# Kernel tuning notes

Hardware: AMD Instinct MI355X
Metric: run time of the kernel (lower is better)

## Reference

```python
import jax, jax.numpy as jnp
import numpy as np

EPS = 1e-3  # keras LayerNormalization default epsilon


def _layernorm(x, gamma, beta):
    mu = jnp.mean(x, axis=-1, keepdims=True)
    var = jnp.mean(jnp.square(x - mu), axis=-1, keepdims=True)
    return (x - mu) * jax.lax.rsqrt(var + EPS) * gamma + beta


def setup_inputs() -> dict:
    key = jax.random.key(0)
    B, T, D, H = 8, 2048, 192, 3
    KD = D           # TalkingHeadsAttention(key_dim=dim, value_dim=dim)
    HID = 4 * D      # mlp_ratio = 4.0
    ks = jax.random.split(key, 12)
    s_in = 0.02
    inp = {
        "x": jax.random.normal(ks[0], (B, T, D), jnp.float32),
        # norm1 / norm2
        "gamma1": jnp.ones((D,), jnp.float32),
        "beta1": jnp.zeros((D,), jnp.float32),
        "gamma2": jnp.ones((D,), jnp.float32),
        "beta2": jnp.zeros((D,), jnp.float32),
        # attention projections (qkv_bias=False -> no biases)
        "wq": jax.random.normal(ks[1], (D, H, KD), jnp.float32) * s_in,
        "wk": jax.random.normal(ks[2], (D, H, KD), jnp.float32) * s_in,
        "wv": jax.random.normal(ks[3], (D, H, KD), jnp.float32) * s_in,
        "wo": jax.random.normal(ks[4], (H, KD, D), jnp.float32) * s_in,
        # talking-heads mixing matrices [H, H]
        "pre_w": jnp.eye(H, dtype=jnp.float32) + jax.random.normal(ks[5], (H, H), jnp.float32) * 0.02,
        "post_w": jnp.eye(H, dtype=jnp.float32) + jax.random.normal(ks[6], (H, H), jnp.float32) * 0.02,
        # MLP (bias=True)
        "w1": jax.random.normal(ks[7], (D, HID), jnp.float32) * s_in,
        "b1": jnp.zeros((HID,), jnp.float32),
        "w2": jax.random.normal(ks[8], (HID, D), jnp.float32) * s_in,
        "b2": jnp.zeros((D,), jnp.float32),
    }
    return inp


def reference(x, gamma1, beta1, gamma2, beta2, wq, wk, wv, wo, pre_w, post_w, w1, b1, w2, b2):
    KD = wq.shape[-1]
    # --- pre-norm + talking-heads attention ---
    n = _layernorm(x, gamma1, beta1)                      # [B,T,D]
    q = jnp.einsum("btd,dhk->bthk", n, wq)               # [B,T,H,KD]
    k = jnp.einsum("bsd,dhk->bshk", n, wk)
    v = jnp.einsum("bsd,dhk->bshk", n, wv)
    scores = jnp.einsum("bthk,bshk->bhts", q, k) / jnp.sqrt(jnp.asarray(KD, x.dtype))
    scores = jnp.einsum("bhts,hg->bgts", scores, pre_w)   # pre-softmax head mix
    probs = jax.nn.softmax(scores, axis=-1)
    probs = jnp.einsum("bhts,hg->bgts", probs, post_w)    # post-softmax head mix
    ctx = jnp.einsum("bhts,bshk->bthk", probs, v)         # [B,T,H,KD]
    attn_out = jnp.einsum("bthk,hkd->btd", ctx, wo)       # [B,T,D]
    x = x + attn_out                                      # ls1/drop_path1 are Identity
    # --- pre-norm + MLP ---
    n2 = _layernorm(x, gamma2, beta2)
    h = jax.nn.gelu(n2 @ w1 + b1, approximate=False)      # keras gelu = exact erf
    mlp_out = h @ w2 + b2
    return x + mlp_out
```

## Files before the change

### kernel.cpp

```cpp
#include <hip/hip_runtime.h>
#include <hip/hip_bf16.h>

typedef __hip_bfloat16 bf16;
typedef unsigned char u8;
typedef __attribute__((ext_vector_type(8))) __bf16 bf16x8;
typedef __attribute__((ext_vector_type(4))) float f32x4;
typedef __attribute__((ext_vector_type(2))) float f32x2;

__device__ __forceinline__ void gld_lds16(const void* g, void* l) {
  __builtin_amdgcn_global_load_lds((const __attribute__((address_space(1))) void*)g,
                                   (__attribute__((address_space(3))) void*)l, 16, 0, 0);
}
__device__ __forceinline__ u8 f2e4m3(float v) {
  return (u8)(__builtin_amdgcn_cvt_pk_fp8_f32(v, 0.f, 0, false) & 0xff);
}
__device__ __forceinline__ f32x2 pk_mul(f32x2 a, f32x2 b) {
  f32x2 d;
  asm("v_pk_mul_f32 %0, %1, %2" : "=v"(d) : "v"(a), "v"(b));
  return d;
}
__device__ __forceinline__ f32x2 pk_fma(f32x2 a, f32x2 b, f32x2 c) {
  f32x2 d;
  asm("v_pk_fma_f32 %0, %1, %2, %3" : "=v"(d) : "v"(a), "v"(b), "v"(c));
  return d;
}

__global__ __launch_bounds__(256) void prep_weights(
    const float* __restrict__ wq, const float* __restrict__ wk,
    const float* __restrict__ w1, const float* __restrict__ w2,
    bf16* __restrict__ WqkvT, bf16* __restrict__ w1T, bf16* __restrict__ w2T)
{
  int i = blockIdx.x * 256 + threadIdx.x;
  if (i < 221184) {
    int n = i / 192, d = i % 192;
    int sel = n / 576, c = n % 576, h = c / 192, kd = c % 192;
    const float* w = (sel == 0) ? wq : wk;
    WqkvT[i] = __float2bfloat16(w[(d*3 + h)*192 + kd]);
    return;
  }
  i -= 221184;
  if (i < 147456) {
    int j = i / 192, d = i % 192;
    w1T[i] = __float2bfloat16(w1[d*768 + j]);
    return;
  }
  i -= 147456;
  if (i < 147456) {
    int d = i / 768, j = i % 768;
    w2T[i] = __float2bfloat16(w2[j*192 + d]);
  }
}

__global__ __launch_bounds__(192) void wm_k(
    const float* __restrict__ wv, const float* __restrict__ wo,
    const float* __restrict__ post_w, bf16* __restrict__ WqkvT)
{
  const int dd = threadIdx.x;
  const int h  = blockIdx.x / 192;
  const int din = blockIdx.x % 192;
  float acc = 0.f;
  #pragma unroll
  for (int g2 = 0; g2 < 3; ++g2) {
    const float pw = post_w[h*3 + g2];
    const float* wvp = wv + (size_t)din*576 + g2*192;
    const float* wop = wo + (size_t)(g2*192)*192 + dd;
    float s = 0.f;
    for (int kd = 0; kd < 192; ++kd)
      s += wvp[kd] * wop[(size_t)kd*192];
    acc += pw * s;
  }
  WqkvT[(size_t)(1152 + h*192 + dd)*192 + din] = __float2bfloat16(acc);
}

__global__ __launch_bounds__(256) void ln_k(const float* __restrict__ x,
    const float* __restrict__ gamma, const float* __restrict__ beta,
    bf16* __restrict__ out)
{
  int row = blockIdx.x * 4 + (threadIdx.x >> 6);
  int lane = threadIdx.x & 63;
  const float* xr = x + (size_t)row * 192;
  float v0 = xr[lane], v1 = xr[lane + 64], v2 = xr[lane + 128];
  float s = v0 + v1 + v2;
  #pragma unroll
  for (int o = 32; o; o >>= 1) s += __shfl_xor(s, o);
  float mu = s * (1.f / 192.f);
  float d0 = v0 - mu, d1 = v1 - mu, d2 = v2 - mu;
  float q = d0*d0 + d1*d1 + d2*d2;
  #pragma unroll
  for (int o = 32; o; o >>= 1) q += __shfl_xor(q, o);
  float rs = rsqrtf(q * (1.f / 192.f) + 1e-3f);
  bf16* orow = out + (size_t)row * 192;
  orow[lane]       = __float2bfloat16(d0*rs*gamma[lane]       + beta[lane]);
  orow[lane + 64]  = __float2bfloat16(d1*rs*gamma[lane + 64]  + beta[lane + 64]);
  orow[lane + 128] = __float2bfloat16(d2*rs*gamma[lane + 128] + beta[lane + 128]);
}

enum { EPI_QKV = 0, EPI_GELU = 3, EPI_OUT = 4 };

template<int EPI, int MROWS = 128>
__global__ __launch_bounds__(256) void gemm_bt(
    const bf16* __restrict__ A, const bf16* __restrict__ BT,
    int M, int N, int K,
    float* __restrict__ outF, bf16* __restrict__ outB,
    const float* __restrict__ bias,
    u8* __restrict__ q_out, u8* __restrict__ k_out, u8* __restrict__ mt_out)
{
  constexpr int MB = MROWS / 32;
  const int tid = threadIdx.x, lane = tid & 63, wid = tid >> 6;
  const int wm = wid >> 1, wn = wid & 1;
  const int row0 = blockIdx.y * MROWS, col0 = blockIdx.x * 64;
  __shared__ __align__(16) bf16 As[2][MROWS * 32];
  __shared__ __align__(16) bf16 Bs[2][64 * 32];
  f32x4 acc[MB][2] = {};
  const int NT = K >> 5;

#define STAGE(buf_, kt_) do { \
    const bf16* Ab_ = A + (size_t)row0 * K + (kt_) * 32; \
    int c0_ = tid, r0_ = c0_ >> 2, cc0_ = (c0_ & 3) << 3; \
    gld_lds16(Ab_ + (size_t)r0_ * K + cc0_, &As[buf_][c0_ * 8]); \
    if constexpr (MROWS == 128) { \
      int c1_ = tid + 256, r1_ = c1_ >> 2, cc1_ = (c1_ & 3) << 3; \
      gld_lds16(Ab_ + (size_t)r1_ * K + cc1_, &As[buf_][c1_ * 8]); \
    } \
    const bf16* Bb_ = BT + (size_t)col0 * K + (kt_) * 32; \
    gld_lds16(Bb_ + (size_t)(tid >> 2) * K + ((tid & 3) << 3), &Bs[buf_][tid * 8]); \
  } while (0)

  STAGE(0, 0);
  for (int kt = 0; kt < NT; ++kt) {
    __syncthreads();
    const int buf = kt & 1;
    if (kt + 1 < NT) STAGE(buf ^ 1, kt + 1);
    const int koff = (lane >> 4) * 8;
    bf16x8 af[MB], bfr[2];
    #pragma unroll
    for (int m = 0; m < MB; ++m)
      af[m] = *(const bf16x8*)&As[buf][(wm*(MROWS/2) + m*16 + (lane & 15))*32 + koff];
    #pragma unroll
    for (int n = 0; n < 2; ++n)
      bfr[n] = *(const bf16x8*)&Bs[buf][(wn*32 + n*16 + (lane & 15))*32 + koff];
    #pragma unroll
    for (int m = 0; m < MB; ++m)
      #pragma unroll
      for (int n = 0; n < 2; ++n)
        acc[m][n] = __builtin_amdgcn_mfma_f32_16x16x32_bf16(af[m], bfr[n], acc[m][n], 0, 0, 0);
  }
#undef STAGE

  const int rbase = row0 + wm * (MROWS/2);
  const int cbase = col0 + wn * 32;
  #pragma unroll
  for (int m = 0; m < MB; ++m) {
    #pragma unroll
    for (int n = 0; n < 2; ++n) {
      const int col = cbase + n*16 + (lane & 15);
      const int rtop = rbase + m*16 + ((lane >> 4) << 2);
      if constexpr (EPI == EPI_QKV) {
        const int b = rtop >> 11, t_ = rtop & 2047;
        const int sel = col / 576, c2 = col % 576;
        const int h = c2 / 192, kd = c2 % 192;
        if (sel == 2) {
          int pk = __builtin_amdgcn_cvt_pk_fp8_f32(acc[m][n][0], acc[m][n][1], 0, false);
          pk = __builtin_amdgcn_cvt_pk_fp8_f32(acc[m][n][2], acc[m][n][3], pk, true);
          const size_t fo = ((((size_t)b*64 + (t_>>5))*3 + h)*12 + (kd>>4))*512
                          + (((kd&15) + (((t_>>3)&3)<<4))<<3) + (t_&4);
          *(unsigned*)&mt_out[fo] = (unsigned)pk;
        } else {
          #pragma unroll
          for (int j = 0; j < 4; ++j) {
            const int t = t_ + j;
            const size_t fo = ((((size_t)b*64 + (t>>5))*3 + h)*6 + (kd>>5))*1024
                            + (((t>>4)&1))*512
                            + (((t&15) + (((kd>>3)&3)<<4))<<3) + (kd&7);
            if (sel == 0) q_out[fo] = f2e4m3(acc[m][n][j]);
            else          k_out[fo] = f2e4m3(acc[m][n][j]);
          }
        }
      } else {
        #pragma unroll
        for (int j = 0; j < 4; ++j) {
          const int row = rtop + j;
          const float v = acc[m][n][j];
          if constexpr (EPI == EPI_GELU) {
            const float u = v + bias[col];
            outB[(size_t)row * 768 + col] =
                __float2bfloat16(0.5f * u * (1.f + erff(u * 0.70710678118654752f)));
          } else if constexpr (EPI == EPI_OUT) {
            const size_t idx = (size_t)row * 192 + col;
            outF[idx] = outF[idx] + v + bias[col];
          }
        }
      }
    }
  }
}

__global__ __launch_bounds__(256, 2) void attn_k(
    const u8* __restrict__ q, const u8* __restrict__ kf,
    const u8* __restrict__ MT, const float* __restrict__ pre_w,
    const float* __restrict__ x, const float* __restrict__ gamma2,
    const float* __restrict__ beta2, float* __restrict__ out,
    bf16* __restrict__ nb)
{
  const int tid = threadIdx.x, lane = tid & 63, wv = tid >> 6;
  const int l15 = lane & 15, l4 = lane >> 4;
  const int tq = wv & 1, sq = wv >> 1;
  const int bid = blockIdx.x;
  const int b = bid & 7;
  const int tt = bid >> 3;
  const int t0 = tt * 32;

  __shared__ __align__(16) u8 Ks[2][18432];
  __shared__ __align__(16) u8 Ps[2][3072];
  __shared__ float rlPart[2][3][32];
  __shared__ float lnS[4][32][2];

  const u8* qfb = q + ((size_t)b*64 + tt) * 18432;
  long qf[3][6];
  #pragma unroll
  for (int h = 0; h < 3; ++h)
    #pragma unroll
    for (int kq = 0; kq < 6; ++kq)
      qf[h][kq] = *(const long*)(qfb + ((h*6 + kq)*2 + tq)*512 + lane*8);

  f32x2 pwf2[9];
  #pragma unroll
  for (int i = 0; i < 9; ++i) {
    const float v = pre_w[i] * 0.07216878364870323f * 1.44269504088896f;
    pwf2[i][0] = v; pwf2[i][1] = v;
  }

  f32x4 acc[3][2][3] = {};
  float sgacc[3] = {0.f, 0.f, 0.f};
  const int trow = tq*16 + l15;
  const int psw = (l15 >> 2) & 3;
  const int pwr = (((sq*2 + (l4 >> 1)) ^ psw) << 3) + ((l4 & 1) << 2);
  const int prd = (l4 ^ psw) << 3;

  const u8* kfb = kf + (size_t)b * 64 * 18432;
  const u8* mtb = MT + (size_t)b * 64 * 18432;

#define STAGEK(buf_, st_) do { \
    const u8* kb_ = kfb + (size_t)(st_) * 18432; \
    _Pragma("unroll") \
    for (int i_ = 0; i_ < 5; ++i_) { \
      const int L_ = i_ * 256 + tid; \
      if (L_ < 1152) gld_lds16(kb_ + L_*16, &Ks[buf_][L_*16]); \
    } \
  } while (0)

#define LOADMF(MF_, st_) do { \
    const u8* mb_ = mtb + (size_t)(st_) * 18432 + wv*3*512 + lane*8; \
    _Pragma("unroll") \
    for (int g_ = 0; g_ < 3; ++g_) \
      _Pragma("unroll") \
      for (int n_ = 0; n_ < 3; ++n_) \
        MF_[g_][n_] = *(const long*)(mb_ + (g_*12 + n_)*512); \
  } while (0)

#define PV(stm1_, MF_) do { \
    const int bp_ = (stm1_) & 1; \
    __builtin_amdgcn_s_setprio(1); \
    _Pragma("unroll") \
    for (int g_ = 0; g_ < 3; ++g_) \
      _Pragma("unroll") \
      for (int m_ = 0; m_ < 2; ++m_) { \
        const long pf_ = *(const long*)&Ps[bp_][g_*1024 + (m_*16 + l15)*32 + prd]; \
        _Pragma("unroll") \
        for (int n_ = 0; n_ < 3; ++n_) \
          acc[g_][m_][n_] = __builtin_amdgcn_mfma_f32_16x16x32_fp8_fp8(pf_, MF_[g_][n_], acc[g_][m_][n_], 0, 0, 0); \
      } \
    __builtin_amdgcn_s_setprio(0); \
  } while (0)

#define QKSM(st_) do { \
    const int bq_ = (st_) & 1; \
    f32x4 sacc0 = {}, sacc1 = {}, sacc2 = {}; \
    __builtin_amdgcn_s_setprio(1); \
    _Pragma("unroll") \
    for (int kq_ = 0; kq_ < 6; ++kq_) { \
      const long kf0_ = *(const long*)&Ks[bq_][((0*6 + kq_)*2 + sq)*512 + lane*8]; \
      sacc0 = __builtin_amdgcn_mfma_f32_16x16x32_fp8_fp8(kf0_, qf[0][kq_], sacc0, 0, 0, 0); \
      const long kf1_ = *(const long*)&Ks[bq_][((1*6 + kq_)*2 + sq)*512 + lane*8]; \
      sacc1 = __builtin_amdgcn_mfma_f32_16x16x32_fp8_fp8(kf1_, qf[1][kq_], sacc1, 0, 0, 0); \
      const long kf2_ = *(const long*)&Ks[bq_][((2*6 + kq_)*2 + sq)*512 + lane*8]; \
      sacc2 = __builtin_amdgcn_mfma_f32_16x16x32_fp8_fp8(kf2_, qf[2][kq_], sacc2, 0, 0, 0); \
    } \
    __builtin_amdgcn_s_setprio(0); \
    f32x2 p0a = {sacc0[0], sacc0[1]}, p0b = {sacc0[2], sacc0[3]}; \
    f32x2 p1a = {sacc1[0], sacc1[1]}, p1b = {sacc1[2], sacc1[3]}; \
    f32x2 p2a = {sacc2[0], sacc2[1]}, p2b = {sacc2[2], sacc2[3]}; \
    _Pragma("unroll") \
    for (int g_ = 0; g_ < 3; ++g_) { \
      f32x2 va = pk_mul(p0a, pwf2[g_]); \
      va = pk_fma(p1a, pwf2[3+g_], va); \
      va = pk_fma(p2a, pwf2[6+g_], va); \
      f32x2 vb = pk_mul(p0b, pwf2[g_]); \
      vb = pk_fma(p1b, pwf2[3+g_], vb); \
      vb = pk_fma(p2b, pwf2[6+g_], vb); \
      float e0_ = exp2f(va[0]), e1_ = exp2f(va[1]); \
      float e2_ = exp2f(vb[0]), e3_ = exp2f(vb[1]); \
      sgacc[g_] += (e0_ + e1_) + (e2_ + e3_); \
      int pk_ = __builtin_amdgcn_cvt_pk_fp8_f32(e0_, e1_, 0, false); \
      pk_ = __builtin_amdgcn_cvt_pk_fp8_f32(e2_, e3_, pk_, true); \
      *(unsigned*)&Ps[bq_][g_*1024 + trow*32 + pwr] = (unsigned)pk_; \
    } \
  } while (0)

  long mfA[3][3], mfB[3][3];

  STAGEK(0, 0);
  __syncthreads();
  STAGEK(1, 1);
  LOADMF(mfA, 0);
  QKSM(0);
  for (int st = 1; st < 63; st += 2) {
    __syncthreads();
    STAGEK((st + 1) & 1, st + 1);
    LOADMF(mfB, st);
    PV(st - 1, mfA);
    QKSM(st);
    __syncthreads();
    if (st + 2 < 64) STAGEK((st + 2) & 1, st + 2);
    LOADMF(mfA, st + 1);
    PV(st, mfB);
    QKSM(st + 1);
  }
  __syncthreads();
  LOADMF(mfB, 63);
  PV(62, mfA);
  QKSM(63);
  __syncthreads();
  PV(63, mfB);
  #pragma unroll
  for (int g = 0; g < 3; ++g) {
    float s = sgacc[g];
    s += __shfl_xor(s, 16);
    s += __shfl_xor(s, 32);
    if (l4 == 0) rlPart[sq][g][trow] = s;
  }
  __syncthreads();

  float ovv[2][3][4];
  #pragma unroll
  for (int m = 0; m < 2; ++m) {
    #pragma unroll
    for (int j = 0; j < 4; ++j) {
      const int row = m*16 + l4*4 + j;
      float rlv[3];
      #pragma unroll
      for (int g = 0; g < 3; ++g)
        rlv[g] = 1.f / (rlPart[0][g][row] + rlPart[1][g][row]);
      float s = 0.f, ss = 0.f;
      #pragma unroll
      for (int n = 0; n < 3; ++n) {
        const int d = wv*48 + n*16 + l15;
        const size_t idx = ((size_t)b*2048 + t0 + row)*192 + d;
        const float ov = x[idx] + rlv[0]*acc[0][m][n][j] + rlv[1]*acc[1][m][n][j]
                                + rlv[2]*acc[2][m][n][j];
        out[idx] = ov;
        ovv[m][n][j] = ov;
        s += ov; ss += ov*ov;
      }
      #pragma unroll
      for (int o = 1; o < 16; o <<= 1) { s += __shfl_xor(s, o); ss += __shfl_xor(ss, o); }
      if (l15 == 0) { lnS[wv][row][0] = s; lnS[wv][row][1] = ss; }
    }
  }
  __syncthreads();

  float gmL[3], btL[3];
  #pragma unroll
  for (int n = 0; n < 3; ++n) {
    const int d = wv*48 + n*16 + l15;
    gmL[n] = gamma2[d]; btL[n] = beta2[d];
  }
  #pragma unroll
  for (int m = 0; m < 2; ++m) {
    #pragma unroll
    for (int j = 0; j < 4; ++j) {
      const int row = m*16 + l4*4 + j;
      const float ts  = lnS[0][row][0] + lnS[1][row][0] + lnS[2][row][0] + lnS[3][row][0];
      const float tss = lnS[0][row][1] + lnS[1][row][1] + lnS[2][row][1] + lnS[3][row][1];
      const float mu = ts * (1.f / 192.f);
      const float rs = rsqrtf(tss * (1.f / 192.f) - mu*mu + 1e-3f);
      #pragma unroll
      for (int n = 0; n < 3; ++n) {
        const int d = wv*48 + n*16 + l15;
        nb[((size_t)b*2048 + t0 + row)*192 + d] =
            __float2bfloat16((ovv[m][n][j] - mu) * rs * gmL[n] + btL[n]);
      }
    }
  }
#undef STAGEK
#undef LOADMF
#undef PV
#undef QKSM
}

extern "C" void kernel_launch(void* const* d_in, const int* in_sizes, int n_in,
                              void* d_out, int out_size, void* d_ws, size_t ws_size,
                              hipStream_t stream)
{
  (void)in_sizes; (void)n_in; (void)out_size; (void)ws_size;
  const float* x      = (const float*)d_in[0];
  const float* gamma1 = (const float*)d_in[1];
  const float* beta1  = (const float*)d_in[2];
  const float* gamma2 = (const float*)d_in[3];
  const float* beta2  = (const float*)d_in[4];
  const float* wq     = (const float*)d_in[5];
  const float* wk     = (const float*)d_in[6];
  const float* wv     = (const float*)d_in[7];
  const float* wo     = (const float*)d_in[8];
  const float* pre_w  = (const float*)d_in[9];
  const float* post_w = (const float*)d_in[10];
  const float* w1     = (const float*)d_in[11];
  const float* b1     = (const float*)d_in[12];
  const float* w2     = (const float*)d_in[13];
  const float* b2     = (const float*)d_in[14];
  float* out = (float*)d_out;

  uint8_t* base = (uint8_t*)d_ws;
  size_t off = 0;
  auto alloc = [&](size_t bytes) {
    uint8_t* r = base + off; off += (bytes + 255) & ~(size_t)255; return r;
  };
  bf16* nb      = (bf16*)alloc((size_t)16384 * 192 * 2);
  u8*   qb      = (u8*)alloc((size_t)9437184);
  u8*   kb      = (u8*)alloc((size_t)9437184);
  u8*   MTslab  = (u8*)alloc((size_t)9437184);
  bf16* WqkvT   = (bf16*)alloc((size_t)331776 * 2);
  bf16* w1T     = (bf16*)alloc((size_t)147456 * 2);
  bf16* w2T     = (bf16*)alloc((size_t)147456 * 2);
  bf16* hb      = (bf16*)qb;

  prep_weights<<<2016, 256, 0, stream>>>(wq, wk, w1, w2, WqkvT, w1T, w2T);
  wm_k<<<576, 192, 0, stream>>>(wv, wo, post_w, WqkvT);
  ln_k<<<4096, 256, 0, stream>>>(x, gamma1, beta1, nb);
  gemm_bt<EPI_QKV, 128><<<dim3(27, 128, 1), 256, 0, stream>>>(nb, WqkvT, 16384, 1728, 192,
      nullptr, nullptr, nullptr, qb, kb, MTslab);
  attn_k<<<512, 256, 0, stream>>>(qb, kb, MTslab, pre_w, x, gamma2, beta2, out, nb);
  gemm_bt<EPI_GELU, 128><<<dim3(12, 128, 1), 256, 0, stream>>>(nb, w1T, 16384, 768, 192,
      nullptr, hb, b1, nullptr, nullptr, nullptr);
  gemm_bt<EPI_OUT, 64><<<dim3(3, 256, 1), 256, 0, stream>>>(hb, w2T, 16384, 192, 768,
      out, nullptr, b2, nullptr, nullptr, nullptr);
}
```

Baseline: 195.8 us.

## Fuse MLP fc1+GELU+fc2 into one kernel keeping hidden activations in LDS

Replaces the two MLP GEMM launches with a single fused kernel. Each block takes 32 rows and loops over 64-wide hidden chunks, computing the fc1 chunk with GELU into LDS and accumulating fc2 directly. This removes the bf16 hidden tensor round trip through global memory and one launch. The w2 weights are pre-swizzled into an MFMA fragment layout so they can be loaded straight into registers. The tradeoffs are that only 512 blocks run with serial per-chunk syncs, and the w1 chunks are re-fetched per block, which may limit occupancy and parallelism.

Result: faster. 186.0 us (-5.0%).

```diff
diff --git a/kernel.cpp b/kernel.cpp
--- a/kernel.cpp
+++ b/kernel.cpp
@@ -28,7 +28,7 @@
 __global__ __launch_bounds__(256) void prep_weights(
     const float* __restrict__ wq, const float* __restrict__ wk,
     const float* __restrict__ w1, const float* __restrict__ w2,
-    bf16* __restrict__ WqkvT, bf16* __restrict__ w1T, bf16* __restrict__ w2T)
+    bf16* __restrict__ WqkvT, bf16* __restrict__ w1T, bf16* __restrict__ w2f)
 {
   int i = blockIdx.x * 256 + threadIdx.x;
   if (i < 221184) {
@@ -46,8 +46,11 @@
   }
   i -= 147456;
   if (i < 147456) {
-    int d = i / 768, j = i % 768;
-    w2T[i] = __float2bfloat16(w2[j*192 + d]);
+    int j = i / 192, d = i % 192;
+    int c = j >> 6, ks = (j >> 5) & 1, l4 = (j >> 3) & 3, e = j & 7;
+    int dn = d >> 4, l15 = d & 15;
+    w2f[(size_t)((((c*2 + ks)*12 + dn)*64) + l4*16 + l15)*8 + e] =
+        __float2bfloat16(w2[(size_t)j*192 + d]);
   }
 }
 
@@ -95,101 +98,173 @@
   orow[lane + 128] = __float2bfloat16(d2*rs*gamma[lane + 128] + beta[lane + 128]);
 }
 
-enum { EPI_QKV = 0, EPI_GELU = 3, EPI_OUT = 4 };
-
-template<int EPI, int MROWS = 128>
-__global__ __launch_bounds__(256) void gemm_bt(
+__global__ __launch_bounds__(256) void gemm_qkv(
     const bf16* __restrict__ A, const bf16* __restrict__ BT,
-    int M, int N, int K,
-    float* __restrict__ outF, bf16* __restrict__ outB,
-    const float* __restrict__ bias,
     u8* __restrict__ q_out, u8* __restrict__ k_out, u8* __restrict__ mt_out)
 {
-  constexpr int MB = MROWS / 32;
+  const int K = 192;
   const int tid = threadIdx.x, lane = tid & 63, wid = tid >> 6;
   const int wm = wid >> 1, wn = wid & 1;
-  const int row0 = blockIdx.y * MROWS, col0 = blockIdx.x * 64;
-  __shared__ __align__(16) bf16 As[2][MROWS * 32];
+  const int row0 = blockIdx.y * 128, col0 = blockIdx.x * 64;
+  __shared__ __align__(16) bf16 As[2][128 * 32];
   __shared__ __align__(16) bf16 Bs[2][64 * 32];
-  f32x4 acc[MB][2] = {};
-  const int NT = K >> 5;
+  f32x4 acc[4][2] = {};
 
 #define STAGE(buf_, kt_) do { \
     const bf16* Ab_ = A + (size_t)row0 * K + (kt_) * 32; \
     int c0_ = tid, r0_ = c0_ >> 2, cc0_ = (c0_ & 3) << 3; \
     gld_lds16(Ab_ + (size_t)r0_ * K + cc0_, &As[buf_][c0_ * 8]); \
-    if constexpr (MROWS == 128) { \
-      int c1_ = tid + 256, r1_ = c1_ >> 2, cc1_ = (c1_ & 3) << 3; \
-      gld_lds16(Ab_ + (size_t)r1_ * K + cc1_, &As[buf_][c1_ * 8]); \
-    } \
+    int c1_ = tid + 256, r1_ = c1_ >> 2, cc1_ = (c1_ & 3) << 3; \
+    gld_lds16(Ab_ + (size_t)r1_ * K + cc1_, &As[buf_][c1_ * 8]); \
     const bf16* Bb_ = BT + (size_t)col0 * K + (kt_) * 32; \
     gld_lds16(Bb_ + (size_t)(tid >> 2) * K + ((tid & 3) << 3), &Bs[buf_][tid * 8]); \
   } while (0)
 
   STAGE(0, 0);
-  for (int kt = 0; kt < NT; ++kt) {
+  for (int kt = 0; kt < 6; ++kt) {
     __syncthreads();
     const int buf = kt & 1;
-    if (kt + 1 < NT) STAGE(buf ^ 1, kt + 1);
+    if (kt + 1 < 6) STAGE(buf ^ 1, kt + 1);
     const int koff = (lane >> 4) * 8;
-    bf16x8 af[MB], bfr[2];
-    #pragma unroll
-    for (int m = 0; m < MB; ++m)
-      af[m] = *(const bf16x8*)&As[buf][(wm*(MROWS/2) + m*16 + (lane & 15))*32 + koff];
+    bf16x8 af[4], bfr[2];
+    #pragma unroll
+    for (int m = 0; m < 4; ++m)
+      af[m] = *(const bf16x8*)&As[buf][(wm*64 + m*16 + (lane & 15))*32 + koff];
     #pragma unroll
     for (int n = 0; n < 2; ++n)
       bfr[n] = *(const bf16x8*)&Bs[buf][(wn*32 + n*16 + (lane & 15))*32 + koff];
     #pragma unroll
-    for (int m = 0; m < MB; ++m)
+    for (int m = 0; m < 4; ++m)
       #pragma unroll
       for (int n = 0; n < 2; ++n)
         acc[m][n] = __builtin_amdgcn_mfma_f32_16x16x32_bf16(af[m], bfr[n], acc[m][n], 0, 0, 0);
   }
 #undef STAGE
 
-  const int rbase = row0 + wm * (MROWS/2);
+  const int rbase = row0 + wm * 64;
   const int cbase = col0 + wn * 32;
   #pragma unroll
-  for (int m = 0; m < MB; ++m) {
+  for (int m = 0; m < 4; ++m) {
     #pragma unroll
     for (int n = 0; n < 2; ++n) {
       const int col = cbase + n*16 + (lane & 15);
       const int rtop = rbase + m*16 + ((lane >> 4) << 2);
-      if constexpr (EPI == EPI_QKV) {
-        const int b = rtop >> 11, t_ = rtop & 2047;
-        const int sel = col / 576, c2 = col % 576;
-        const int h = c2 / 192, kd = c2 % 192;
-        if (sel == 2) {
-          int pk = __builtin_amdgcn_cvt_pk_fp8_f32(acc[m][n][0], acc[m][n][1], 0, false);
-          pk = __builtin_amdgcn_cvt_pk_fp8_f32(acc[m][n][2], acc[m][n][3], pk, true);
-          const size_t fo = ((((size_t)b*64 + (t_>>5))*3 + h)*12 + (kd>>4))*512
-                          + (((kd&15) + (((t_>>3)&3)<<4))<<3) + (t_&4);
-          *(unsigned*)&mt_out[fo] = (unsigned)pk;
-        } else {
-          #pragma unroll
-          for (int j = 0; j < 4; ++j) {
-            const int t = t_ + j;
-            const size_t fo = ((((size_t)b*64 + (t>>5))*3 + h)*6 + (kd>>5))*1024
-                            + (((t>>4)&1))*512
-                            + (((t&15) + (((kd>>3)&3)<<4))<<3) + (kd&7);
-            if (sel == 0) q_out[fo] = f2e4m3(acc[m][n][j]);
-            else          k_out[fo] = f2e4m3(acc[m][n][j]);
-          }
-        }
+      const int b = rtop >> 11, t_ = rtop & 2047;
+      const int sel = col / 576, c2 = col % 576;
+      const int h = c2 / 192, kd = c2 % 192;
+      if (sel == 2) {
+        int pk = __builtin_amdgcn_cvt_pk_fp8_f32(acc[m][n][0], acc[m][n][1], 0, false);
+        pk = __builtin_amdgcn_cvt_pk_fp8_f32(acc[m][n][2], acc[m][n][3], pk, true);
+        const size_t fo = ((((size_t)b*64 + (t_>>5))*3 + h)*12 + (kd>>4))*512
+                        + (((kd&15) + (((t_>>3)&3)<<4))<<3) + (t_&4);
+        *(unsigned*)&mt_out[fo] = (unsigned)pk;
       } else {
         #pragma unroll
         for (int j = 0; j < 4; ++j) {
-          const int row = rtop + j;
-          const float v = acc[m][n][j];
-          if constexpr (EPI == EPI_GELU) {
-            const float u = v + bias[col];
-            outB[(size_t)row * 768 + col] =
-                __float2bfloat16(0.5f * u * (1.f + erff(u * 0.70710678118654752f)));
-          } else if constexpr (EPI == EPI_OUT) {
-            const size_t idx = (size_t)row * 192 + col;
-            outF[idx] = outF[idx] + v + bias[col];
-          }
+          const int t = t_ + j;
+          const size_t fo = ((((size_t)b*64 + (t>>5))*3 + h)*6 + (kd>>5))*1024
+                          + (((t>>4)&1))*512
+                          + (((t&15) + (((kd>>3)&3)<<4))<<3) + (kd&7);
+          if (sel == 0) q_out[fo] = f2e4m3(acc[m][n][j]);
+          else          k_out[fo] = f2e4m3(acc[m][n][j]);
         }
+      }
+    }
+  }
+}
+
+__global__ __launch_bounds__(256, 2) void mlp_k(
+    const bf16* __restrict__ nb, const bf16* __restrict__ w1T,
+    const bf16* __restrict__ w2f, const float* __restrict__ b1,
+    const float* __restrict__ b2, float* __restrict__ out)
+{
+  const int tid = threadIdx.x, lane = tid & 63, w = tid >> 6;
+  const int l15 = lane & 15, l4 = lane >> 4;
+  const int wm = w >> 1, wn = w & 1;
+  const int row0 = blockIdx.x * 32;
+
+  __shared__ __align__(16) bf16 As[6 * 32 * 32];
+  __shared__ __align__(16) bf16 Bs[6 * 64 * 32];
+  __shared__ __align__(16) bf16 Hs[32 * 72];
+
+  #pragma unroll
+  for (int i = 0; i < 3; ++i) {
+    const int L = i * 256 + tid;
+    const int kq = L >> 7, rem = L & 127, r = rem >> 2, sp = rem & 3;
+    gld_lds16(nb + (size_t)(row0 + r) * 192 + kq*32 + sp*8, &As[L * 8]);
+  }
+#define STAGEB(c_) do { \
+    _Pragma("unroll") \
+    for (int i_ = 0; i_ < 6; ++i_) { \
+      const int L_ = i_ * 256 + tid; \
+      const int kq_ = L_ >> 8, rem_ = L_ & 255, r_ = rem_ >> 2, sp_ = rem_ & 3; \
+      gld_lds16(w1T + (size_t)((c_)*64 + r_) * 192 + kq_*32 + sp_*8, &Bs[L_ * 8]); \
+    } \
+  } while (0)
+
+  STAGEB(0);
+  __syncthreads();
+
+  f32x4 acc[2][3] = {};
+  for (int c = 0; c < 12; ++c) {
+    bf16x8 wf[3][2];
+    #pragma unroll
+    for (int n = 0; n < 3; ++n)
+      #pragma unroll
+      for (int ks = 0; ks < 2; ++ks)
+        wf[n][ks] = *(const bf16x8*)(w2f + (size_t)((((c*2 + ks)*12) + w*3 + n)*64 + lane)*8);
+
+    f32x4 sacc[2] = {};
+    const int koff = l4*8;
+    #pragma unroll
+    for (int kq = 0; kq < 6; ++kq) {
+      const bf16x8 af = *(const bf16x8*)&As[(kq*32 + wm*16 + l15)*32 + koff];
+      #pragma unroll
+      for (int n = 0; n < 2; ++n) {
+        const bf16x8 bfr = *(const bf16x8*)&Bs[(kq*64 + wn*32 + n*16 + l15)*32 + koff];
+        sacc[n] = __builtin_amdgcn_mfma_f32_16x16x32_bf16(af, bfr, sacc[n], 0, 0, 0);
+      }
+    }
+    #pragma unroll
+    for (int n = 0; n < 2; ++n) {
+      const int jc = wn*32 + n*16 + l15;
+      const float bv = b1[c*64 + jc];
+      #pragma unroll
+      for (int jr = 0; jr < 4; ++jr) {
+        const float u = sacc[n][jr] + bv;
+        const float g = 0.5f * u * (1.f + erff(u * 0.70710678118654752f));
+        Hs[(wm*16 + l4*4 + jr)*72 + jc] = __float2bfloat16(g);
+      }
+    }
+    __syncthreads();
+    if (c + 1 < 12) STAGEB(c + 1);
+    #pragma unroll
+    for (int ks = 0; ks < 2; ++ks) {
+      bf16x8 ha[2];
+      #pragma unroll
+      for (int m = 0; m < 2; ++m)
+        ha[m] = *(const bf16x8*)&Hs[(m*16 + l15)*72 + ks*32 + l4*8];
+      #pragma unroll
+      for (int m = 0; m < 2; ++m)
+        #pragma unroll
+        for (int n = 0; n < 3; ++n)
+          acc[m][n] = __builtin_amdgcn_mfma_f32_16x16x32_bf16(ha[m], wf[n][ks], acc[m][n], 0, 0, 0);
+    }
+    __syncthreads();
+  }
+#undef STAGEB
+
+  #pragma unroll
+  for (int n = 0; n < 3; ++n) {
+    const int d = w*48 + n*16 + l15;
+    const float b2v = b2[d];
+    #pragma unroll
+    for (int m = 0; m < 2; ++m) {
+      #pragma unroll
+      for (int jr = 0; jr < 4; ++jr) {
+        const int t = m*16 + l4*4 + jr;
+        const size_t idx = (size_t)(row0 + t)*192 + d;
+        out[idx] = out[idx] + acc[m][n][jr] + b2v;
       }
     }
   }
@@ -431,17 +506,12 @@
   u8*   MTslab  = (u8*)alloc((size_t)9437184);
   bf16* WqkvT   = (bf16*)alloc((size_t)331776 * 2);
   bf16* w1T     = (bf16*)alloc((size_t)147456 * 2);
-  bf16* w2T     = (bf16*)alloc((size_t)147456 * 2);
-  bf16* hb      = (bf16*)qb;
-
-  prep_weights<<<2016, 256, 0, stream>>>(wq, wk, w1, w2, WqkvT, w1T, w2T);
+  bf16* w2f     = (bf16*)alloc((size_t)147456 * 2);
+
+  prep_weights<<<2016, 256, 0, stream>>>(wq, wk, w1, w2, WqkvT, w1T, w2f);
   wm_k<<<576, 192, 0, stream>>>(wv, wo, post_w, WqkvT);
   ln_k<<<4096, 256, 0, stream>>>(x, gamma1, beta1, nb);
-  gemm_bt<EPI_QKV, 128><<<dim3(27, 128, 1), 256, 0, stream>>>(nb, WqkvT, 16384, 1728, 192,
-      nullptr, nullptr, nullptr, qb, kb, MTslab);
+  gemm_qkv<<<dim3(27, 128, 1), 256, 0, stream>>>(nb, WqkvT, qb, kb, MTslab);
   attn_k<<<512, 256, 0, stream>>>(qb, kb, MTslab, pre_w, x, gamma2, beta2, out, nb);
-  gemm_bt<EPI_GELU, 128><<<dim3(12, 128, 1), 256, 0, stream>>>(nb, w1T, 16384, 768, 192,
-      nullptr, hb, b1, nullptr, nullptr, nullptr);
-  gemm_bt<EPI_OUT, 64><<<dim3(3, 256, 1), 256, 0, stream>>>(hb, w2T, 16384, 192, 768,
-      out, nullptr, b2, nullptr, nullptr, nullptr);
-}
+  mlp_k<<<512, 256, 0, stream>>>(nb, w1T, w2f, b1, b2, out);
+}
```
